# Kernel optimization log

Measured on AMD Instinct MI355X. Metric: run time of the kernel, lower is better.

Reference implementation:

```python
import jax, jax.numpy as jnp
import numpy as np

# dims: batch, q-heads, kv-heads, seq, head_dim, block size, window (kv blocks per q block)
B, H, KVH, S, D = 2, 16, 4, 4096, 64
BLK, W = 64, 8
G = H // KVH          # heads per group = 4
NQ = S // BLK         # 64 query blocks
L = W * BLK           # flattened kv window per q block = 512


def setup_inputs() -> dict:
    key = jax.random.key(0)
    k0, k1, k2, k3 = jax.random.split(key, 4)
    q = jax.random.normal(k0, (B, H, S, D), jnp.float32)
    k = jax.random.normal(k1, (B, KVH, S, D), jnp.float32)
    v = jax.random.normal(k2, (B, KVH, S, D), jnp.float32)
    # standard alibi slopes 2^(-8i/H)
    alibi_slopes = jnp.asarray(2.0 ** (-8.0 * np.arange(1, H + 1) / H), jnp.float32)
    # contiguous segments via sorted random ids
    segment_ids = jnp.sort(jax.random.randint(k3, (B, S), 0, 8, jnp.int32), axis=-1)
    # causal sliding window: q block qb attends to kv blocks [qb-W+1, qb]; -1 = invalid
    qb = np.arange(NQ)[:, None]
    bi = qb - (W - 1) + np.arange(W)[None, :]
    block_indices = jnp.asarray(np.where(bi < 0, -1, bi), jnp.int32)  # [NQ, W]
    return {"q": q, "k": k, "v": v, "alibi_slopes": alibi_slopes,
            "segment_ids": segment_ids, "block_indices": block_indices}


def reference(q, k, v, alibi_slopes, segment_ids, block_indices):
    scale = jnp.float32(1.0 / np.sqrt(D))
    NEG = jnp.float32(-1e30)

    qg = q.reshape(B, KVH, G, NQ, BLK, D)          # GQA grouping
    kb = k.reshape(B, KVH, NQ, BLK, D)
    vb = v.reshape(B, KVH, NQ, BLK, D)

    safe = jnp.clip(block_indices, 0)               # [NQ, W]
    kg = kb[:, :, safe]                             # [B,KVH,NQ,W,BLK,D] gathered kv blocks
    vg = vb[:, :, safe]

    pos_m = (jnp.arange(NQ) * BLK)[:, None] + jnp.arange(BLK)             # [NQ,BM]
    pos_n = safe[:, :, None] * BLK + jnp.arange(BLK)[None, None, :]       # [NQ,W,BN]

    valid = (block_indices >= 0)[:, None, :, None]                        # [NQ,1,W,1]
    causal = pos_m[:, :, None, None] >= pos_n[:, None, :, :]              # [NQ,BM,W,BN]
    seg_q = segment_ids.reshape(B, NQ, BLK)
    seg_k = jnp.take(segment_ids, pos_n.reshape(-1), axis=1).reshape(B, NQ, W, BLK)
    same_seg = (seg_q[:, :, :, None, None] == seg_k[:, :, None, :, :]) & (seg_q[:, :, :, None, None] >= 0)
    mask = ((valid & causal)[None] & same_seg)                            # [B,NQ,BM,W,BN]
    maskb = mask.reshape(B, 1, 1, NQ, BLK, L)                             # broadcast over KVH,G

    scores = jnp.einsum('bkgqmd,bkqwnd->bkgqmwn', qg, kg) * scale         # [B,KVH,G,NQ,BM,W,BN]
    pos_diff = jnp.abs(pos_m[:, :, None, None] - pos_n[:, None, :, :]).astype(jnp.float32)
    scores = scores - alibi_slopes.reshape(KVH, G)[None, :, :, None, None, None, None] * pos_diff
    scores = scores.reshape(B, KVH, G, NQ, BLK, L)
    scores = jnp.where(maskb, scores, NEG)

    row_max = jnp.max(scores, axis=-1, keepdims=True)
    p = jnp.where(maskb, jnp.exp(scores - row_max), 0.0)
    l = jnp.sum(p, axis=-1, keepdims=True)                                # [B,KVH,G,NQ,BM,1]
    vf = vg.reshape(B, KVH, NQ, L, D)
    acc = jnp.einsum('bkgqml,bkqld->bkgqmd', p, vf)
    out = jnp.where(l > 0, acc / jnp.where(l > 0, l, 1.0), 0.0)           # zero rows with no valid kv
    return out.reshape(B, H, S, D)
```

## Files before the change

kernel.cpp:

```cpp
#include <hip/hip_runtime.h>
#include <hip/hip_bf16.h>

#define NKVH 4
#define SEQ 4096
#define BLK 64
#define NW 8
#define NQB 64

typedef __attribute__((ext_vector_type(8))) short bf16x8;
typedef __attribute__((ext_vector_type(4))) float f32x4;

__device__ __forceinline__ unsigned pkbf(unsigned lo, unsigned hi) {
  return __builtin_amdgcn_perm(hi + 0x8000u, lo + 0x8000u, 0x07060302u);
}

__device__ __forceinline__ void gload16(const void* g, void* l) {
  __builtin_amdgcn_global_load_lds(
      (const __attribute__((address_space(1))) void*)g,
      (__attribute__((address_space(3))) void*)l, 16, 0, 0);
}

__global__ __launch_bounds__(256, 2)
void prep_kernel(const float* __restrict__ kp, const float* __restrict__ vp,
                 const int* __restrict__ seg,
                 short* __restrict__ kw, short* __restrict__ vt,
                 int* __restrict__ fo)
{
  const int ki = blockIdx.x, kvh = blockIdx.y, b = blockIdx.z;
  const size_t base = (((size_t)(b*NKVH + kvh)*SEQ) + (size_t)ki*BLK)*64;
  __shared__ float sk[64][72];
  __shared__ float sv[64][72];
  const int t = threadIdx.x;
  #pragma unroll
  for (int it = 0; it < 4; ++it) {
    const int i = t + it*256;
    const int row = i >> 4, c4 = i & 15;
    float4 a = *(const float4*)(kp + base + row*64 + c4*4);
    *(float4*)&sk[row][c4*4] = a;
    float4 v = *(const float4*)(vp + base + row*64 + c4*4);
    *(float4*)&sv[row][c4*4] = v;
  }
  if (kvh == 0 && t < BLK) {
    const int idx = ki*BLK + t;
    const int v = seg[b*SEQ + idx];
    const bool bnd = (idx == 0) || (seg[b*SEQ + idx - 1] != v);
    if (bnd) fo[b*8 + v] = idx;
  }
  __syncthreads();
  #pragma unroll
  for (int it = 0; it < 2; ++it) {
    const int o = t + it*256;
    const int s = o >> 8, fd = (o >> 6) & 3, lg = (o >> 4) & 3, lr = o & 15;
    const int krow = 8*(lr >> 2) + (lr & 3) + 4*(fd & 1) + 32*(fd >> 1);
    const float* src = &sk[krow][s*32 + lg*8];
    uint4 w;
    w.x = pkbf(__float_as_uint(src[0]), __float_as_uint(src[1]));
    w.y = pkbf(__float_as_uint(src[2]), __float_as_uint(src[3]));
    w.z = pkbf(__float_as_uint(src[4]), __float_as_uint(src[5]));
    w.w = pkbf(__float_as_uint(src[6]), __float_as_uint(src[7]));
    *(uint4*)(kw + base + (size_t)o*8) = w;
    const int d = fd*16 + lr;
    const int n0 = s*32 + lg*8;
    uint4 u;
    u.x = pkbf(__float_as_uint(sv[n0+0][d]), __float_as_uint(sv[n0+1][d]));
    u.y = pkbf(__float_as_uint(sv[n0+2][d]), __float_as_uint(sv[n0+3][d]));
    u.z = pkbf(__float_as_uint(sv[n0+4][d]), __float_as_uint(sv[n0+5][d]));
    u.w = pkbf(__float_as_uint(sv[n0+6][d]), __float_as_uint(sv[n0+7][d]));
    *(uint4*)(vt + base + (size_t)o*8) = u;
  }
}

__global__ __launch_bounds__(256, 2)
void sattn_kernel(const float* __restrict__ qp, const short* __restrict__ kw,
                  const short* __restrict__ vt, const float* __restrict__ alibi,
                  const int* __restrict__ seg, const int* __restrict__ bidx,
                  const int* __restrict__ fo, float* __restrict__ outp)
{
  const int raw = blockIdx.x;
  const int xcd = raw & 7, li = raw >> 3;
  const int b = xcd >> 2, kvh = xcd & 3;
  const int qb = li & 63, hp = li >> 6;

  const int tid = threadIdx.x;
  const int wave = tid >> 6, lane = tid & 63;
  const int lr = lane & 15, lg = lane >> 4;
  const int wh = wave & 1, wq = wave >> 1;
  const int head = kvh*4 + hp*2 + wh;

  __shared__ short klds[4][4096];
  __shared__ short vlds[4][4096];

  int kis[NW];
  #pragma unroll
  for (int i = 0; i < NW; ++i) kis[i] = bidx[qb*NW + i];

  int m_glob[2], lo[2];
  unsigned relm[2];
  #pragma unroll
  for (int g = 0; g < 2; ++g) {
    m_glob[g] = qb*BLK + (wq*2 + g)*16 + lr;
    const int sv = seg[b*SEQ + m_glob[g]];
    lo[g] = fo[b*8 + sv];
    relm[g] = (unsigned)(m_glob[g] - lo[g]);
  }
  const float LOG2E = 1.4426950408889634f;
  const float nslope = -alibi[head] * LOG2E;

  float A2[2], cnr[4][4];
  #pragma unroll
  for (int g = 0; g < 2; ++g) A2[g] = nslope * (float)m_glob[g];
  #pragma unroll
  for (int f = 0; f < 4; ++f) {
    const int nb = lg*8 + 4*(f & 1) + 32*(f >> 1);
    #pragma unroll
    for (int r = 0; r < 4; ++r) cnr[f][r] = nslope * (float)(nb + r);
  }

  const short* kbase = kw + ((size_t)(b*NKVH + kvh)*SEQ)*64;
  const short* vbase = vt + ((size_t)(b*NKVH + kvh)*SEQ)*64;

  auto STAGE = [&](int buf, int wi) {
    const int ki = kis[wi] < 0 ? 0 : kis[wi];
    const char* ksrc = (const char*)(kbase + (size_t)ki*4096);
    const char* vsrc = (const char*)(vbase + (size_t)ki*4096);
    gload16(ksrc + tid*16,        (char*)&klds[buf][0] + wave*1024);
    gload16(ksrc + 4096 + tid*16, (char*)&klds[buf][0] + 4096 + wave*1024);
    gload16(vsrc + tid*16,        (char*)&vlds[buf][0] + wave*1024);
    gload16(vsrc + 4096 + tid*16, (char*)&vlds[buf][0] + 4096 + wave*1024);
  };

  STAGE(0, 0);
  STAGE(1, 1);

  bf16x8 qf[2][2];
  {
    const float qs = 0.125f * LOG2E;
    #pragma unroll
    for (int g = 0; g < 2; ++g) {
      const float* qrow = qp + (((size_t)b*16 + head)*SEQ + m_glob[g])*64;
      #pragma unroll
      for (int s = 0; s < 2; ++s) {
        float4 a = *(const float4*)(qrow + s*32 + lg*8);
        float4 c = *(const float4*)(qrow + s*32 + lg*8 + 4);
        union { unsigned u[4]; bf16x8 v; } cv;
        cv.u[0] = pkbf(__float_as_uint(a.x*qs), __float_as_uint(a.y*qs));
        cv.u[1] = pkbf(__float_as_uint(a.z*qs), __float_as_uint(a.w*qs));
        cv.u[2] = pkbf(__float_as_uint(c.x*qs), __float_as_uint(c.y*qs));
        cv.u[3] = pkbf(__float_as_uint(c.z*qs), __float_as_uint(c.w*qs));
        qf[g][s] = cv.v;
      }
    }
  }

  union { unsigned short us[8]; bf16x8 v; } one_u;
  #pragma unroll
  for (int i = 0; i < 8; ++i) one_u.us[i] = 0x3F80;
  const bf16x8 onesf = one_u.v;

  f32x4 oacc[2][4], osum[2];
  #pragma unroll
  for (int g = 0; g < 2; ++g) {
    f32x4 z = {0.f,0.f,0.f,0.f};
    osum[g] = z;
    #pragma unroll
    for (int dt = 0; dt < 4; ++dt) oacc[g][dt] = z;
  }

  asm volatile("s_waitcnt vmcnt(0)" ::: "memory");
  __builtin_amdgcn_s_barrier();

  #pragma unroll
  for (int t2 = 0; t2 < 4; ++t2) {
    if (t2 < 3) {
      STAGE((2*t2 + 2) & 3, 2*t2 + 2);
      STAGE((2*t2 + 3) & 3, 2*t2 + 3);
    }
    #pragma unroll
    for (int w = 0; w < 2; ++w) {
      const int wi = 2*t2 + w;
      const int kvi = kis[wi];
      if (kvi >= 0) {
        const float B = nslope * (float)(kvi*BLK);
        const bool fast = (wi != NW-1) &&
            __all((kvi*BLK >= lo[0]) && (kvi*BLK >= lo[1]));

        f32x4 sacc[2][4];
        #pragma unroll
        for (int g = 0; g < 2; ++g) {
          const float Dg = A2[g] - B;
          #pragma unroll
          for (int f = 0; f < 4; ++f)
            #pragma unroll
            for (int r = 0; r < 4; ++r) sacc[g][f][r] = Dg - cnr[f][r];
        }
        #pragma unroll
        for (int s = 0; s < 2; ++s) {
          bf16x8 kf[4];
          #pragma unroll
          for (int f = 0; f < 4; ++f)
            kf[f] = *(const bf16x8*)&klds[wi & 3][(s*256 + f*64 + lane)*8];
          __builtin_amdgcn_s_setprio(1);
          #pragma unroll
          for (int f = 0; f < 4; ++f)
            sacc[0][f] = __builtin_amdgcn_mfma_f32_16x16x32_bf16(kf[f], qf[0][s], sacc[0][f], 0, 0, 0);
          #pragma unroll
          for (int f = 0; f < 4; ++f)
            sacc[1][f] = __builtin_amdgcn_mfma_f32_16x16x32_bf16(kf[f], qf[1][s], sacc[1][f], 0, 0, 0);
          __builtin_amdgcn_s_setprio(0);
        }

        union { unsigned u[4]; bf16x8 v; } pfs[2][2];
        if (fast) {
          #pragma unroll
          for (int g = 0; g < 2; ++g)
            #pragma unroll
            for (int f = 0; f < 4; ++f) {
              const float p0 = __builtin_amdgcn_exp2f(sacc[g][f][0]);
              const float p1 = __builtin_amdgcn_exp2f(sacc[g][f][1]);
              const float p2 = __builtin_amdgcn_exp2f(sacc[g][f][2]);
              const float p3 = __builtin_amdgcn_exp2f(sacc[g][f][3]);
              pfs[g][f >> 1].u[(f & 1)*2 + 0] = pkbf(__float_as_uint(p0), __float_as_uint(p1));
              pfs[g][f >> 1].u[(f & 1)*2 + 1] = pkbf(__float_as_uint(p2), __float_as_uint(p3));
            }
        } else {
          #pragma unroll
          for (int g = 0; g < 2; ++g)
            #pragma unroll
            for (int f = 0; f < 4; ++f) {
              const int nb = lg*8 + 4*(f & 1) + 32*(f >> 1);
              const unsigned nrel0 = (unsigned)(kvi*BLK + nb - lo[g]);
              float p[4];
              #pragma unroll
              for (int r = 0; r < 4; ++r) {
                const bool live = (nrel0 + (unsigned)r) <= relm[g];
                const float pv = __builtin_amdgcn_exp2f(sacc[g][f][r]);
                p[r] = live ? pv : 0.f;
              }
              pfs[g][f >> 1].u[(f & 1)*2 + 0] = pkbf(__float_as_uint(p[0]), __float_as_uint(p[1]));
              pfs[g][f >> 1].u[(f & 1)*2 + 1] = pkbf(__float_as_uint(p[2]), __float_as_uint(p[3]));
            }
        }

        #pragma unroll
        for (int s = 0; s < 2; ++s) {
          bf16x8 vf[4];
          #pragma unroll
          for (int dt = 0; dt < 4; ++dt)
            vf[dt] = *(const bf16x8*)&vlds[wi & 3][(s*256 + dt*64 + lane)*8];
          __builtin_amdgcn_s_setprio(1);
          #pragma unroll
          for (int dt = 0; dt < 4; ++dt)
            oacc[0][dt] = __builtin_amdgcn_mfma_f32_16x16x32_bf16(vf[dt], pfs[0][s].v, oacc[0][dt], 0, 0, 0);
          #pragma unroll
          for (int dt = 0; dt < 4; ++dt)
            oacc[1][dt] = __builtin_amdgcn_mfma_f32_16x16x32_bf16(vf[dt], pfs[1][s].v, oacc[1][dt], 0, 0, 0);
          osum[0] = __builtin_amdgcn_mfma_f32_16x16x32_bf16(onesf, pfs[0][s].v, osum[0], 0, 0, 0);
          osum[1] = __builtin_amdgcn_mfma_f32_16x16x32_bf16(onesf, pfs[1][s].v, osum[1], 0, 0, 0);
          __builtin_amdgcn_s_setprio(0);
        }
      }
    }
    if (t2 < 3) {
      asm volatile("s_waitcnt vmcnt(0)" ::: "memory");
      __builtin_amdgcn_s_barrier();
    }
  }

  #pragma unroll
  for (int g = 0; g < 2; ++g) {
    const float lrow = osum[g][0];
    const float inv = lrow > 0.f ? 1.f/lrow : 0.f;
    float* dst = outp + (((size_t)b*16 + head)*SEQ + m_glob[g])*64;
    #pragma unroll
    for (int dt = 0; dt < 4; ++dt) {
      float4 o;
      o.x = oacc[g][dt][0]*inv; o.y = oacc[g][dt][1]*inv;
      o.z = oacc[g][dt][2]*inv; o.w = oacc[g][dt][3]*inv;
      *(float4*)&dst[dt*16 + lg*4] = o;
    }
  }
}

extern "C" void kernel_launch(void* const* d_in, const int* in_sizes, int n_in,
                              void* d_out, int out_size, void* d_ws, size_t ws_size,
                              hipStream_t stream) {
  const float* q    = (const float*)d_in[0];
  const float* k    = (const float*)d_in[1];
  const float* v    = (const float*)d_in[2];
  const float* al   = (const float*)d_in[3];
  const int*   sg   = (const int*)d_in[4];
  const int*   bi   = (const int*)d_in[5];
  short* kws  = (short*)d_ws;
  short* vtws = (short*)((char*)d_ws + (size_t)(1u<<22));
  int*   fo   = (int*)((char*)d_ws + (size_t)(1u<<23));
  dim3 pgrid(NQB, NKVH, 2);
  prep_kernel<<<pgrid, 256, 0, stream>>>(k, v, sg, kws, vtws, fo);
  sattn_kernel<<<dim3(1024), 256, 0, stream>>>(q, kws, vtws, al, sg, bi, fo, (float*)d_out);
}
```

Baseline: 45.91 us.

## Split KV window across two wave groups and merge partial outputs via LDS

Doubles the block to 512 threads so that two groups of four waves each process half of the 8-block KV window for the same query rows. Each group keeps its own double-buffered K/V tiles in LDS, and the partial accumulators and row sums are combined through shared memory before normalisation. The aim is a shorter serial chain per wave and more waves in flight to hide load and MFMA latency. In exchange it adds a reduction step with two extra barriers, and the register limit per thread is tighter because of the 512-thread launch bound. Skipping the max subtraction across the two halves stays valid because the softmax has no running max.

```diff
diff --git a/kernel.cpp b/kernel.cpp
--- a/kernel.cpp
+++ b/kernel.cpp
@@ -70,7 +70,7 @@
   }
 }
 
-__global__ __launch_bounds__(256, 2)
+__global__ __launch_bounds__(512, 2)
 void sattn_kernel(const float* __restrict__ qp, const short* __restrict__ kw,
                   const short* __restrict__ vt, const float* __restrict__ alibi,
                   const int* __restrict__ seg, const int* __restrict__ bidx,
@@ -84,15 +84,17 @@
   const int tid = threadIdx.x;
   const int wave = tid >> 6, lane = tid & 63;
   const int lr = lane & 15, lg = lane >> 4;
-  const int wh = wave & 1, wq = wave >> 1;
-  const int head = kvh*4 + hp*2 + wh;
-
-  __shared__ short klds[4][4096];
-  __shared__ short vlds[4][4096];
-
-  int kis[NW];
-  #pragma unroll
-  for (int i = 0; i < NW; ++i) kis[i] = bidx[qb*NW + i];
+  const int half = wave >> 2, sub = wave & 3;
+  const int hh = sub & 1, wq = sub >> 1;
+  const int head = kvh*4 + hp*2 + hh;
+  const int tloc = tid & 255, wloc = (tid >> 6) & 3;
+
+  __shared__ short klds[2][2][4096];
+  __shared__ short vlds[2][2][4096];
+
+  int kis[4];
+  #pragma unroll
+  for (int i = 0; i < 4; ++i) kis[i] = bidx[qb*NW + half*4 + i];
 
   int m_glob[2], lo[2];
   unsigned relm[2];
@@ -119,18 +121,19 @@
   const short* kbase = kw + ((size_t)(b*NKVH + kvh)*SEQ)*64;
   const short* vbase = vt + ((size_t)(b*NKVH + kvh)*SEQ)*64;
 
-  auto STAGE = [&](int buf, int wi) {
-    const int ki = kis[wi] < 0 ? 0 : kis[wi];
+  auto STAGE = [&](int buf, int j) {
+    const int ki = kis[j] < 0 ? 0 : kis[j];
     const char* ksrc = (const char*)(kbase + (size_t)ki*4096);
     const char* vsrc = (const char*)(vbase + (size_t)ki*4096);
-    gload16(ksrc + tid*16,        (char*)&klds[buf][0] + wave*1024);
-    gload16(ksrc + 4096 + tid*16, (char*)&klds[buf][0] + 4096 + wave*1024);
-    gload16(vsrc + tid*16,        (char*)&vlds[buf][0] + wave*1024);
-    gload16(vsrc + 4096 + tid*16, (char*)&vlds[buf][0] + 4096 + wave*1024);
+    char* kdst = (char*)&klds[half][buf][0];
+    char* vdst = (char*)&vlds[half][buf][0];
+    gload16(ksrc + tloc*16,        kdst + wloc*1024);
+    gload16(ksrc + 4096 + tloc*16, kdst + 4096 + wloc*1024);
+    gload16(vsrc + tloc*16,        vdst + wloc*1024);
+    gload16(vsrc + 4096 + tloc*16, vdst + 4096 + wloc*1024);
   };
 
   STAGE(0, 0);
-  STAGE(1, 1);
 
   bf16x8 qf[2][2];
   {
@@ -170,113 +173,134 @@
   __builtin_amdgcn_s_barrier();
 
   #pragma unroll
-  for (int t2 = 0; t2 < 4; ++t2) {
-    if (t2 < 3) {
-      STAGE((2*t2 + 2) & 3, 2*t2 + 2);
-      STAGE((2*t2 + 3) & 3, 2*t2 + 3);
+  for (int j = 0; j < 4; ++j) {
+    if (j < 3) STAGE((j + 1) & 1, j + 1);
+    const int kvi = kis[j];
+    if (kvi >= 0) {
+      const int wiG = half*4 + j;
+      const float B = nslope * (float)(kvi*BLK);
+      const bool fast = (wiG != NW-1) &&
+          __all((kvi*BLK >= lo[0]) && (kvi*BLK >= lo[1]));
+
+      f32x4 sacc[2][4];
+      #pragma unroll
+      for (int g = 0; g < 2; ++g) {
+        const float Dg = A2[g] - B;
+        #pragma unroll
+        for (int f = 0; f < 4; ++f)
+          #pragma unroll
+          for (int r = 0; r < 4; ++r) sacc[g][f][r] = Dg - cnr[f][r];
+      }
+      #pragma unroll
+      for (int s = 0; s < 2; ++s) {
+        bf16x8 kf[4];
+        #pragma unroll
+        for (int f = 0; f < 4; ++f)
+          kf[f] = *(const bf16x8*)&klds[half][j & 1][(s*256 + f*64 + lane)*8];
+        __builtin_amdgcn_s_setprio(1);
+        #pragma unroll
+        for (int f = 0; f < 4; ++f)
+          sacc[0][f] = __builtin_amdgcn_mfma_f32_16x16x32_bf16(kf[f], qf[0][s], sacc[0][f], 0, 0, 0);
+        #pragma unroll
+        for (int f = 0; f < 4; ++f)
+          sacc[1][f] = __builtin_amdgcn_mfma_f32_16x16x32_bf16(kf[f], qf[1][s], sacc[1][f], 0, 0, 0);
+        __builtin_amdgcn_s_setprio(0);
+      }
+
+      union { unsigned u[4]; bf16x8 v; } pfs[2][2];
+      if (fast) {
+        #pragma unroll
+        for (int g = 0; g < 2; ++g)
+          #pragma unroll
+          for (int f = 0; f < 4; ++f) {
+            const float p0 = __builtin_amdgcn_exp2f(sacc[g][f][0]);
+            const float p1 = __builtin_amdgcn_exp2f(sacc[g][f][1]);
+            const float p2 = __builtin_amdgcn_exp2f(sacc[g][f][2]);
+            const float p3 = __builtin_amdgcn_exp2f(sacc[g][f][3]);
+            pfs[g][f >> 1].u[(f & 1)*2 + 0] = pkbf(__float_as_uint(p0), __float_as_uint(p1));
+            pfs[g][f >> 1].u[(f & 1)*2 + 1] = pkbf(__float_as_uint(p2), __float_as_uint(p3));
+          }
+      } else {
+        #pragma unroll
+        for (int g = 0; g < 2; ++g)
+          #pragma unroll
+          for (int f = 0; f < 4; ++f) {
+            const int nb = lg*8 + 4*(f & 1) + 32*(f >> 1);
+            const unsigned nrel0 = (unsigned)(kvi*BLK + nb - lo[g]);
+            float p[4];
+            #pragma unroll
+            for (int r = 0; r < 4; ++r) {
+              const bool live = (nrel0 + (unsigned)r) <= relm[g];
+              const float pv = __builtin_amdgcn_exp2f(sacc[g][f][r]);
+              p[r] = live ? pv : 0.f;
+            }
+            pfs[g][f >> 1].u[(f & 1)*2 + 0] = pkbf(__float_as_uint(p[0]), __float_as_uint(p[1]));
+            pfs[g][f >> 1].u[(f & 1)*2 + 1] = pkbf(__float_as_uint(p[2]), __float_as_uint(p[3]));
+          }
+      }
+
+      #pragma unroll
+      for (int s = 0; s < 2; ++s) {
+        bf16x8 vf[4];
+        #pragma unroll
+        for (int dt = 0; dt < 4; ++dt)
+          vf[dt] = *(const bf16x8*)&vlds[half][j & 1][(s*256 + dt*64 + lane)*8];
+        __builtin_amdgcn_s_setprio(1);
+        #pragma unroll
+        for (int dt = 0; dt < 4; ++dt)
+          oacc[0][dt] = __builtin_amdgcn_mfma_f32_16x16x32_bf16(vf[dt], pfs[0][s].v, oacc[0][dt], 0, 0, 0);
+        #pragma unroll
+        for (int dt = 0; dt < 4; ++dt)
+          oacc[1][dt] = __builtin_amdgcn_mfma_f32_16x16x32_bf16(vf[dt], pfs[1][s].v, oacc[1][dt], 0, 0, 0);
+        osum[0] = __builtin_amdgcn_mfma_f32_16x16x32_bf16(onesf, pfs[0][s].v, osum[0], 0, 0, 0);
+        osum[1] = __builtin_amdgcn_mfma_f32_16x16x32_bf16(onesf, pfs[1][s].v, osum[1], 0, 0, 0);
+        __builtin_amdgcn_s_setprio(0);
+      }
     }
-    #pragma unroll
-    for (int w = 0; w < 2; ++w) {
-      const int wi = 2*t2 + w;
-      const int kvi = kis[wi];
-      if (kvi >= 0) {
-        const float B = nslope * (float)(kvi*BLK);
-        const bool fast = (wi != NW-1) &&
-            __all((kvi*BLK >= lo[0]) && (kvi*BLK >= lo[1]));
-
-        f32x4 sacc[2][4];
-        #pragma unroll
-        for (int g = 0; g < 2; ++g) {
-          const float Dg = A2[g] - B;
-          #pragma unroll
-          for (int f = 0; f < 4; ++f)
-            #pragma unroll
-            for (int r = 0; r < 4; ++r) sacc[g][f][r] = Dg - cnr[f][r];
-        }
-        #pragma unroll
-        for (int s = 0; s < 2; ++s) {
-          bf16x8 kf[4];
-          #pragma unroll
-          for (int f = 0; f < 4; ++f)
-            kf[f] = *(const bf16x8*)&klds[wi & 3][(s*256 + f*64 + lane)*8];
-          __builtin_amdgcn_s_setprio(1);
-          #pragma unroll
-          for (int f = 0; f < 4; ++f)
-            sacc[0][f] = __builtin_amdgcn_mfma_f32_16x16x32_bf16(kf[f], qf[0][s], sacc[0][f], 0, 0, 0);
-          #pragma unroll
-          for (int f = 0; f < 4; ++f)
-            sacc[1][f] = __builtin_amdgcn_mfma_f32_16x16x32_bf16(kf[f], qf[1][s], sacc[1][f], 0, 0, 0);
-          __builtin_amdgcn_s_setprio(0);
-        }
-
-        union { unsigned u[4]; bf16x8 v; } pfs[2][2];
-        if (fast) {
-          #pragma unroll
-          for (int g = 0; g < 2; ++g)
-            #pragma unroll
-            for (int f = 0; f < 4; ++f) {
-              const float p0 = __builtin_amdgcn_exp2f(sacc[g][f][0]);
-              const float p1 = __builtin_amdgcn_exp2f(sacc[g][f][1]);
-              const float p2 = __builtin_amdgcn_exp2f(sacc[g][f][2]);
-              const float p3 = __builtin_amdgcn_exp2f(sacc[g][f][3]);
-              pfs[g][f >> 1].u[(f & 1)*2 + 0] = pkbf(__float_as_uint(p0), __float_as_uint(p1));
-              pfs[g][f >> 1].u[(f & 1)*2 + 1] = pkbf(__float_as_uint(p2), __float_as_uint(p3));
-            }
-        } else {
-          #pragma unroll
-          for (int g = 0; g < 2; ++g)
-            #pragma unroll
-            for (int f = 0; f < 4; ++f) {
-              const int nb = lg*8 + 4*(f & 1) + 32*(f >> 1);
-              const unsigned nrel0 = (unsigned)(kvi*BLK + nb - lo[g]);
-              float p[4];
-              #pragma unroll
-              for (int r = 0; r < 4; ++r) {
-                const bool live = (nrel0 + (unsigned)r) <= relm[g];
-                const float pv = __builtin_amdgcn_exp2f(sacc[g][f][r]);
-                p[r] = live ? pv : 0.f;
-              }
-              pfs[g][f >> 1].u[(f & 1)*2 + 0] = pkbf(__float_as_uint(p[0]), __float_as_uint(p[1]));
-              pfs[g][f >> 1].u[(f & 1)*2 + 1] = pkbf(__float_as_uint(p[2]), __float_as_uint(p[3]));
-            }
-        }
-
-        #pragma unroll
-        for (int s = 0; s < 2; ++s) {
-          bf16x8 vf[4];
-          #pragma unroll
-          for (int dt = 0; dt < 4; ++dt)
-            vf[dt] = *(const bf16x8*)&vlds[wi & 3][(s*256 + dt*64 + lane)*8];
-          __builtin_amdgcn_s_setprio(1);
-          #pragma unroll
-          for (int dt = 0; dt < 4; ++dt)
-            oacc[0][dt] = __builtin_amdgcn_mfma_f32_16x16x32_bf16(vf[dt], pfs[0][s].v, oacc[0][dt], 0, 0, 0);
-          #pragma unroll
-          for (int dt = 0; dt < 4; ++dt)
-            oacc[1][dt] = __builtin_amdgcn_mfma_f32_16x16x32_bf16(vf[dt], pfs[1][s].v, oacc[1][dt], 0, 0, 0);
-          osum[0] = __builtin_amdgcn_mfma_f32_16x16x32_bf16(onesf, pfs[0][s].v, osum[0], 0, 0, 0);
-          osum[1] = __builtin_amdgcn_mfma_f32_16x16x32_bf16(onesf, pfs[1][s].v, osum[1], 0, 0, 0);
-          __builtin_amdgcn_s_setprio(0);
-        }
-      }
-    }
-    if (t2 < 3) {
+    if (j < 3) {
       asm volatile("s_waitcnt vmcnt(0)" ::: "memory");
       __builtin_amdgcn_s_barrier();
     }
   }
 
-  #pragma unroll
-  for (int g = 0; g < 2; ++g) {
-    const float lrow = osum[g][0];
-    const float inv = lrow > 0.f ? 1.f/lrow : 0.f;
-    float* dst = outp + (((size_t)b*16 + head)*SEQ + m_glob[g])*64;
-    #pragma unroll
-    for (int dt = 0; dt < 4; ++dt) {
-      float4 o;
-      o.x = oacc[g][dt][0]*inv; o.y = oacc[g][dt][1]*inv;
-      o.z = oacc[g][dt][2]*inv; o.w = oacc[g][dt][3]*inv;
-      *(float4*)&dst[dt*16 + lg*4] = o;
+  __syncthreads();
+  float* cl_o = (float*)&klds[0][0][0];
+  float* cl_s = (float*)&vlds[0][0][0];
+  const int slot = sub*64 + lane;
+  if (half == 1) {
+    #pragma unroll
+    for (int g = 0; g < 2; ++g)
+      #pragma unroll
+      for (int dt = 0; dt < 4; ++dt)
+        #pragma unroll
+        for (int r = 0; r < 4; ++r)
+          cl_o[slot*32 + ((g*16 + dt*4 + r + lane) & 31)] = oacc[g][dt][r];
+    cl_s[slot*2 + 0] = osum[0][0];
+    cl_s[slot*2 + 1] = osum[1][0];
+  }
+  __syncthreads();
+  if (half == 0) {
+    #pragma unroll
+    for (int g = 0; g < 2; ++g)
+      #pragma unroll
+      for (int dt = 0; dt < 4; ++dt)
+        #pragma unroll
+        for (int r = 0; r < 4; ++r)
+          oacc[g][dt][r] += cl_o[slot*32 + ((g*16 + dt*4 + r + lane) & 31)];
+    const float l0 = osum[0][0] + cl_s[slot*2 + 0];
+    const float l1 = osum[1][0] + cl_s[slot*2 + 1];
+    const float lr2[2] = {l0, l1};
+    #pragma unroll
+    for (int g = 0; g < 2; ++g) {
+      const float inv = lr2[g] > 0.f ? 1.f/lr2[g] : 0.f;
+      float* dst = outp + (((size_t)b*16 + head)*SEQ + m_glob[g])*64;
+      #pragma unroll
+      for (int dt = 0; dt < 4; ++dt) {
+        float4 o;
+        o.x = oacc[g][dt][0]*inv; o.y = oacc[g][dt][1]*inv;
+        o.z = oacc[g][dt][2]*inv; o.w = oacc[g][dt][3]*inv;
+        *(float4*)&dst[dt*16 + lg*4] = o;
+      }
     }
   }
 }
@@ -295,5 +319,5 @@
   int*   fo   = (int*)((char*)d_ws + (size_t)(1u<<23));
   dim3 pgrid(NQB, NKVH, 2);
   prep_kernel<<<pgrid, 256, 0, stream>>>(k, v, sg, kws, vtws, fo);
-  sattn_kernel<<<dim3(1024), 256, 0, stream>>>(q, kws, vtws, al, sg, bi, fo, (float*)d_out);
-}
+  sattn_kernel<<<dim3(1024), 512, 0, stream>>>(q, kws, vtws, al, sg, bi, fo, (float*)d_out);
+}
```

Measured after the change: 55.20 us. +20.2%, slower.
